# Kernel optimization log

Measured on AMD Instinct MI355X. Metric: run time of the kernel, lower is better.

## Reference

```python
import jax, jax.numpy as jnp
import numpy as np

N = 50000      # number of nodes in batch
K = 32         # padded max neighbors
D = 100        # emb_dim
V = 500000     # n_items
LAYERS = 2


def setup_inputs() -> dict:
    key = jax.random.key(0)
    ks = jax.random.split(key, 9)
    nodes = jax.random.randint(ks[0], (N,), 0, V)
    nei = jax.random.randint(ks[1], (N, K), 0, V)          # padded neighbor ids (pad = 0)
    wei = jax.random.uniform(ks[2], (N, K), dtype=jnp.float32)  # edge weights (pad = 0 in real data)
    s_vec = jax.random.normal(ks[3], (N, D), dtype=jnp.float32)
    emb = jax.random.normal(ks[4], (V, D), dtype=jnp.float32) * 0.02
    emb = emb.at[0].set(0.0)                               # padding_idx=0
    W1_w = jax.random.normal(ks[5], (D + 1, D), dtype=jnp.float32) / np.sqrt(D + 1).astype(np.float32)
    W1_b = jnp.zeros((D,), dtype=jnp.float32)
    q1_w = jax.random.normal(ks[6], (D,), dtype=jnp.float32) / np.sqrt(D).astype(np.float32)
    W2_w = jax.random.normal(ks[7], (2 * D, D), dtype=jnp.float32) / np.sqrt(2 * D).astype(np.float32)
    W2_b = jnp.zeros((D,), dtype=jnp.float32)
    return {"nodes": nodes, "nei": nei, "wei": wei, "s_vec": s_vec,
            "emb": emb, "W1_w": W1_w, "W1_b": W1_b, "q1_w": q1_w,
            "W2_w": W2_w, "W2_b": W2_b}


def reference(nodes, nei, wei, s_vec, emb, W1_w, W1_b, q1_w, W2_w, W2_b):
    # x: [N, D] embeddings of the batch nodes
    x = emb[nodes]
    # In the torch code nei/wei are rebuilt identically every layer and h_nei always
    # comes from the frozen embedding table, so the attention message `msg` is
    # layer-invariant; compute it once (same math as the original loop).
    h_nei = emb[nei]                                              # [N, K, D]
    feat = jnp.concatenate([h_nei * s_vec[:, None, :], wei[..., None]], axis=-1)  # [N, K, D+1]
    score = jnp.einsum('nkd,d->nk', jnp.tanh(feat @ W1_w + W1_b), q1_w)           # [N, K]
    att = jax.nn.softmax(score, axis=-1)                          # no masking, as in original
    msg = jnp.einsum('nk,nkd->nd', att, h_nei)                    # [N, D]
    for _ in range(LAYERS):
        x = jax.nn.relu(jnp.concatenate([x, msg], axis=-1) @ W2_w + W2_b)
    return x
```

## Files before the change

kernel.cpp:

```cpp
#include <hip/hip_runtime.h>
#include <cstdint>
#include <cstddef>

typedef __attribute__((ext_vector_type(8))) short bf16x8;
typedef __attribute__((ext_vector_type(16))) float f32x16;

__device__ __forceinline__ unsigned short f2bf(float f) {
    unsigned int u = __builtin_bit_cast(unsigned int, f);
    u += 0x7fffu + ((u >> 16) & 1u);
    return (unsigned short)(u >> 16);
}

__device__ __forceinline__ unsigned int pk2(float a, float b) {
#if __has_builtin(__builtin_amdgcn_cvt_pk_bf16_f32)
    auto r = __builtin_amdgcn_cvt_pk_bf16_f32(a, b);
    return __builtin_bit_cast(unsigned int, r);
#else
    return (unsigned int)f2bf(a) | ((unsigned int)f2bf(b) << 16);
#endif
}

template<int CTRL>
__device__ __forceinline__ float dpp_add(float v) {
    int t = __builtin_amdgcn_update_dpp(0, __builtin_bit_cast(int, v), CTRL, 0xf, 0xf, true);
    return v + __builtin_bit_cast(float, t);
}

__device__ __forceinline__ float fast_tanh(float x) {
    float e = __expf(2.0f * x);
    return 1.0f - 2.0f / (e + 1.0f);
}

__global__ void prep_kernel(const float* __restrict__ W1, const float* __restrict__ W2,
                            unsigned short* __restrict__ W1t, unsigned short* __restrict__ W2t)
{
    int idx = blockIdx.x * 256 + threadIdx.x;
    if (idx < 128 * 128) {
        int nn = idx >> 7, kk = idx & 127;
        W1t[idx] = (nn < 100 && kk < 100) ? f2bf(W1[kk * 100 + nn]) : (unsigned short)0;
    } else {
        int j = idx - 128 * 128;
        if (j < 128 * 208) {
            int nn = j / 208, kk = j - nn * 208;
            unsigned short v = 0;
            if (nn < 100) {
                if (kk < 100) v = f2bf(W2[kk * 100 + nn]);
                else if (kk >= 104 && kk < 204) v = f2bf(W2[(kk - 4) * 100 + nn]);
            }
            W2t[j] = v;
        }
    }
}

#define HP 104
#define P2P 104

__global__ __launch_bounds__(256) void fused_kernel(
    const int* __restrict__ nodes, const int* __restrict__ nei,
    const float* __restrict__ wei, const float* __restrict__ s_vec,
    const float* __restrict__ emb, const float* __restrict__ W1,
    const float* __restrict__ b1, const float* __restrict__ q1,
    const unsigned short* __restrict__ W1t, const unsigned short* __restrict__ W2t,
    const float* __restrict__ b2, float* __restrict__ out, int N)
{
    __shared__ __align__(16) unsigned short h_s[32 * HP];
    __shared__ __align__(16) unsigned short hst[14 * 32 * 8];
    __shared__ __align__(16) unsigned short msg_s[32 * HP];
    __shared__ __align__(16) float part2[16 * P2P];
    __shared__ __align__(16) float spart[4 * 32];
    __shared__ __align__(16) float wei_s[32];

    const int tid  = threadIdx.x;
    const int lane = tid & 63;
    const int w    = tid >> 6;
    const int col  = lane & 31;
    const int hi   = lane >> 5;
    const int n    = w * 32 + col;
    const int n0   = blockIdx.x * 32;

    bf16x8 Bf1[7];
    #pragma unroll
    for (int ks = 0; ks < 7; ++ks)
        Bf1[ks] = *(const bf16x8*)(W1t + n * 128 + ks * 16 + hi * 8);
    const bool nok   = (n < 100);
    const float b1v  = nok ? b1[n] : 0.0f;
    const float w100 = nok ? W1[100 * 100 + n] : 0.0f;
    const float q1v  = nok ? q1[n] : 0.0f;

    if (tid < 32) {
        *(uint2*)&hst[(12 * 32 + tid) * 8 + 4] = make_uint2(0, 0);
        *(uint4*)&hst[(13 * 32 + tid) * 8]     = make_uint4(0, 0, 0, 0);
        *(uint2*)&h_s[tid * HP + 100]          = make_uint2(0, 0);
        *(uint2*)&msg_s[tid * HP + 100]        = make_uint2(0, 0);
    }
    __syncthreads();

    const int gk = tid >> 3;
    const int gj = tid & 7;

    int   nidx_nx = 0;
    float wv_nx   = 0.0f;
    if (n0 < N) {
        nidx_nx = nei[(size_t)n0 * 32 + gk];
        if (tid < 32) wv_nx = wei[(size_t)n0 * 32 + tid];
    }

    for (int it = 0; it < 32; ++it) {
        const int node = n0 + it;
        if (node >= N) break;
        const int   nidx = nidx_nx;
        const float wv   = wv_nx;
        if (it + 1 < 32 && node + 1 < N) {
            nidx_nx = nei[(size_t)(node + 1) * 32 + gk];
            if (tid < 32) wv_nx = wei[(size_t)(node + 1) * 32 + tid];
        }

        {
            if (tid < 32) wei_s[tid] = wv;
            const float4* erow = (const float4*)(emb + (size_t)nidx * 100);
            const float4* srow = (const float4*)(s_vec + (size_t)node * 100);
            float4 h0 = erow[gj],      s0 = srow[gj];
            float4 h1 = erow[gj + 8],  s1 = srow[gj + 8];
            float4 h2 = erow[gj + 16], s2 = srow[gj + 16];
            float4 h3, s3;
            const bool t24 = (gj == 0);
            if (t24) { h3 = erow[24]; s3 = srow[24]; }
            #define ST_C4(c4, h4, s4) { \
                *(uint2*)&h_s[gk * HP + (c4) * 4] = \
                    make_uint2(pk2(h4.x, h4.y), pk2(h4.z, h4.w)); \
                *(uint2*)&hst[(((c4) >> 1) * 32 + gk) * 8 + ((c4) & 1) * 4] = \
                    make_uint2(pk2(h4.x * s4.x, h4.y * s4.y), pk2(h4.z * s4.z, h4.w * s4.w)); }
            ST_C4(gj,      h0, s0)
            ST_C4(gj + 8,  h1, s1)
            ST_C4(gj + 16, h2, s2)
            if (t24) { ST_C4(24, h3, s3) }
            #undef ST_C4
        }
        __syncthreads();

        f32x16 acc;
        #pragma unroll
        for (int q = 0; q < 4; ++q) {
            float4 wq = *(const float4*)&wei_s[q * 8 + hi * 4];
            acc[q * 4 + 0] = fmaf(wq.x, w100, b1v);
            acc[q * 4 + 1] = fmaf(wq.y, w100, b1v);
            acc[q * 4 + 2] = fmaf(wq.z, w100, b1v);
            acc[q * 4 + 3] = fmaf(wq.w, w100, b1v);
        }
        #pragma unroll
        for (int ks = 0; ks < 7; ++ks) {
            bf16x8 a = *(const bf16x8*)&hst[((2 * ks + hi) * 32 + col) * 8];
            acc = __builtin_amdgcn_mfma_f32_32x32x16_bf16(a, Bf1[ks], acc, 0, 0, 0);
        }

        float sv[16];
        #pragma unroll
        for (int r = 0; r < 16; ++r) sv[r] = fast_tanh(acc[r]) * q1v;
        #pragma unroll
        for (int r = 0; r < 16; ++r) {
            float v = sv[r];
            v = dpp_add<0x111>(v);
            v = dpp_add<0x112>(v);
            v = dpp_add<0x114>(v);
            v = dpp_add<0x118>(v);
            v = dpp_add<0x142>(v);
            sv[r] = v;
        }
        if (col == 31) {
            #pragma unroll
            for (int q = 0; q < 4; ++q)
                *(float4*)&spart[w * 32 + q * 8 + hi * 4] =
                    make_float4(sv[q * 4], sv[q * 4 + 1], sv[q * 4 + 2], sv[q * 4 + 3]);
        }
        __syncthreads();

        float attk;
        {
            float s = spart[col] + spart[32 + col] + spart[64 + col] + spart[96 + col];
            float mx = s;
            #pragma unroll
            for (int off = 16; off; off >>= 1) mx = fmaxf(mx, __shfl_xor(mx, off));
            float e = __expf(s - mx);
            float den = e;
            #pragma unroll
            for (int off = 16; off; off >>= 1) den += __shfl_xor(den, off);
            float attv = e / den;
            attk = __shfl(attv, w * 8 + (lane >> 3));
        }

        {
            const int oct  = lane & 7;
            const int krow = w * 8 + (lane >> 3);
            const float a  = attk;
            uint4 r1 = *(const uint4*)&h_s[krow * HP + oct * 8];
            const int oct2 = (oct < 5) ? oct : 4;
            uint4 r2 = *(const uint4*)&h_s[krow * HP + 64 + oct2 * 8];
            float m1[8], m2[8];
            #define UNP2(u, d0, d1) { d0 = __builtin_bit_cast(float, (u) << 16); \
                                      d1 = __builtin_bit_cast(float, (u) & 0xffff0000u); }
            { float t0,t1; UNP2(r1.x,t0,t1); m1[0]=a*t0; m1[1]=a*t1; }
            { float t0,t1; UNP2(r1.y,t0,t1); m1[2]=a*t0; m1[3]=a*t1; }
            { float t0,t1; UNP2(r1.z,t0,t1); m1[4]=a*t0; m1[5]=a*t1; }
            { float t0,t1; UNP2(r1.w,t0,t1); m1[6]=a*t0; m1[7]=a*t1; }
            { float t0,t1; UNP2(r2.x,t0,t1); m2[0]=a*t0; m2[1]=a*t1; }
            { float t0,t1; UNP2(r2.y,t0,t1); m2[2]=a*t0; m2[3]=a*t1; }
            { float t0,t1; UNP2(r2.z,t0,t1); m2[4]=a*t0; m2[5]=a*t1; }
            { float t0,t1; UNP2(r2.w,t0,t1); m2[6]=a*t0; m2[7]=a*t1; }
            #undef UNP2
            #pragma unroll
            for (int j = 0; j < 8; ++j) {
                m1[j] = dpp_add<0x128>(m1[j]);
                m2[j] = dpp_add<0x128>(m2[j]);
            }
            if ((lane & 8) == 0) {
                const int slot = w * 4 + (lane >> 4);
                float* p = &part2[slot * P2P];
                *(float4*)&p[oct * 8]     = make_float4(m1[0], m1[1], m1[2], m1[3]);
                *(float4*)&p[oct * 8 + 4] = make_float4(m1[4], m1[5], m1[6], m1[7]);
                if (oct < 5) {
                    *(float4*)&p[64 + oct * 8]     = make_float4(m2[0], m2[1], m2[2], m2[3]);
                    *(float4*)&p[64 + oct * 8 + 4] = make_float4(m2[4], m2[5], m2[6], m2[7]);
                }
            }
        }
        __syncthreads();

        if (w < 2) {
            int d = w * 64 + lane;
            if (d < 100) {
                float s = 0.0f;
                #pragma unroll
                for (int sl = 0; sl < 16; ++sl) s += part2[sl * P2P + d];
                msg_s[it * HP + d] = f2bf(s);
            }
        }
    }

    __syncthreads();

    bf16x8 Bf2[13];
    #pragma unroll
    for (int ks = 0; ks < 13; ++ks)
        Bf2[ks] = *(const bf16x8*)(W2t + n * 208 + ks * 16 + hi * 8);
    const float b2v = nok ? b2[n] : 0.0f;
    {
        int row = n0 + gk;
        int rc = row < N ? row : N - 1;
        const float4* xr = (const float4*)(emb + (size_t)nodes[rc] * 100);
        float4 x0 = xr[gj], x1 = xr[gj + 8], x2 = xr[gj + 16];
        float4 x3; const bool t24 = (gj == 0);
        if (t24) x3 = xr[24];
        *(uint2*)&h_s[gk * HP + gj * 4]        = make_uint2(pk2(x0.x, x0.y), pk2(x0.z, x0.w));
        *(uint2*)&h_s[gk * HP + (gj + 8) * 4]  = make_uint2(pk2(x1.x, x1.y), pk2(x1.z, x1.w));
        *(uint2*)&h_s[gk * HP + (gj + 16) * 4] = make_uint2(pk2(x2.x, x2.y), pk2(x2.z, x2.w));
        if (t24)
            *(uint2*)&h_s[gk * HP + 96]        = make_uint2(pk2(x3.x, x3.y), pk2(x3.z, x3.w));
    }
    __syncthreads();

    #define AFRAG(ks) (*(const bf16x8*)( \
        (ks) < 6  ? &h_s[col * HP + (ks) * 16 + hi * 8] : \
        (ks) == 6 ? (hi ? &msg_s[col * HP] : &h_s[col * HP + 96]) : \
                    &msg_s[col * HP + (ks) * 16 + hi * 8 - 104]))

    f32x16 acc;
    #pragma unroll
    for (int r = 0; r < 16; ++r) acc[r] = b2v;
    #pragma unroll
    for (int ks = 0; ks < 13; ++ks)
        acc = __builtin_amdgcn_mfma_f32_32x32x16_bf16(AFRAG(ks), Bf2[ks], acc, 0, 0, 0);
    __syncthreads();
    if (nok) {
        #pragma unroll
        for (int r = 0; r < 16; ++r) {
            int m = (r & 3) + 8 * (r >> 2) + 4 * hi;
            h_s[m * HP + n] = f2bf(fmaxf(acc[r], 0.0f));
        }
    }
    __syncthreads();

    f32x16 acc2;
    #pragma unroll
    for (int r = 0; r < 16; ++r) acc2[r] = b2v;
    #pragma unroll
    for (int ks = 0; ks < 13; ++ks)
        acc2 = __builtin_amdgcn_mfma_f32_32x32x16_bf16(AFRAG(ks), Bf2[ks], acc2, 0, 0, 0);
    #undef AFRAG
    if (nok) {
        #pragma unroll
        for (int r = 0; r < 16; ++r) {
            int m = (r & 3) + 8 * (r >> 2) + 4 * hi;
            int row = n0 + m;
            if (row < N) out[(size_t)row * 100 + n] = fmaxf(acc2[r], 0.0f);
        }
    }
}

extern "C" void kernel_launch(void* const* d_in, const int* in_sizes, int n_in,
                              void* d_out, int out_size, void* d_ws, size_t ws_size,
                              hipStream_t stream) {
    const int*   nodes = (const int*)d_in[0];
    const int*   nei   = (const int*)d_in[1];
    const float* wei   = (const float*)d_in[2];
    const float* s_vec = (const float*)d_in[3];
    const float* emb   = (const float*)d_in[4];
    const float* W1    = (const float*)d_in[5];
    const float* b1    = (const float*)d_in[6];
    const float* q1    = (const float*)d_in[7];
    const float* W2    = (const float*)d_in[8];
    const float* b2    = (const float*)d_in[9];
    float* out = (float*)d_out;
    const int N = in_sizes[0];

    unsigned short* W1t = (unsigned short*)d_ws;
    unsigned short* W2t = W1t + 128 * 128;

    prep_kernel<<<168, 256, 0, stream>>>(W1, W2, W1t, W2t);
    const int gB = (N + 31) / 32;
    fused_kernel<<<gB, 256, 0, stream>>>(nodes, nei, wei, s_vec, emb, W1, b1, q1,
                                         W1t, W2t, b2, out, N);
}
```

Baseline: 678.5 us.

## Prefetch next node's neighbor rows into registers and swap MFMA operands for in-lane score reduction

Gathered embedding and s_vec rows for the next node are now loaded into registers during the current iteration, so the global gather overlaps with the attention compute instead of stalling at the start of each iteration. The W1 MFMA operands are swapped so each lane holds scores for one neighbor, which turns the score reduction into an in-lane FMA chain plus a single cross-half shuffle. Message partials are reduced further with swizzle and shuffle steps, so only four LDS slots are written and summed instead of sixteen. The cost is higher register pressure from the prefetched float4s and the per-row bias, weight and q1 arrays, which may reduce occupancy.

```diff
diff --git a/kernel.cpp b/kernel.cpp
--- a/kernel.cpp
+++ b/kernel.cpp
@@ -23,6 +23,11 @@
 template<int CTRL>
 __device__ __forceinline__ float dpp_add(float v) {
     int t = __builtin_amdgcn_update_dpp(0, __builtin_bit_cast(int, v), CTRL, 0xf, 0xf, true);
+    return v + __builtin_bit_cast(float, t);
+}
+
+__device__ __forceinline__ float swz16_add(float v) {
+    int t = __builtin_amdgcn_ds_swizzle(__builtin_bit_cast(int, v), 0x401F);
     return v + __builtin_bit_cast(float, t);
 }
 
@@ -53,7 +58,6 @@
 }
 
 #define HP 104
-#define P2P 104
 
 __global__ __launch_bounds__(256) void fused_kernel(
     const int* __restrict__ nodes, const int* __restrict__ nei,
@@ -66,8 +70,8 @@
     __shared__ __align__(16) unsigned short h_s[32 * HP];
     __shared__ __align__(16) unsigned short hst[14 * 32 * 8];
     __shared__ __align__(16) unsigned short msg_s[32 * HP];
-    __shared__ __align__(16) float part2[16 * P2P];
-    __shared__ __align__(16) float spart[4 * 32];
+    __shared__ __align__(16) float part2[4 * 100];
+    __shared__ __align__(16) float spart[128];
     __shared__ __align__(16) float wei_s[32];
 
     const int tid  = threadIdx.x;
@@ -82,10 +86,17 @@
     #pragma unroll
     for (int ks = 0; ks < 7; ++ks)
         Bf1[ks] = *(const bf16x8*)(W1t + n * 128 + ks * 16 + hi * 8);
-    const bool nok   = (n < 100);
-    const float b1v  = nok ? b1[n] : 0.0f;
-    const float w100 = nok ? W1[100 * 100 + n] : 0.0f;
-    const float q1v  = nok ? q1[n] : 0.0f;
+
+    float b1r[16], w100r[16], q1r[16];
+    #pragma unroll
+    for (int r = 0; r < 16; ++r) {
+        int nn = w * 32 + (r & 3) + 8 * (r >> 2) + 4 * hi;
+        bool ok = nn < 100;
+        b1r[r]   = ok ? b1[nn] : 0.0f;
+        w100r[r] = ok ? W1[100 * 100 + nn] : 0.0f;
+        q1r[r]   = ok ? q1[nn] : 0.0f;
+    }
+    const bool nok = (n < 100);
 
     if (tid < 32) {
         *(uint2*)&hst[(12 * 32 + tid) * 8 + 4] = make_uint2(0, 0);
@@ -93,38 +104,33 @@
         *(uint2*)&h_s[tid * HP + 100]          = make_uint2(0, 0);
         *(uint2*)&msg_s[tid * HP + 100]        = make_uint2(0, 0);
     }
-    __syncthreads();
 
     const int gk = tid >> 3;
     const int gj = tid & 7;
-
-    int   nidx_nx = 0;
-    float wv_nx   = 0.0f;
-    if (n0 < N) {
-        nidx_nx = nei[(size_t)n0 * 32 + gk];
-        if (tid < 32) wv_nx = wei[(size_t)n0 * 32 + tid];
-    }
+    const bool t24 = (gj == 0);
+
+    float4 h0, h1, h2, h3, s0, s1, s2, s3;
+    int   nidx_pf = 0;
+    float wv = 0.0f;
+    {
+        int nid0 = nei[(size_t)n0 * 32 + gk];
+        const float4* erow = (const float4*)(emb + (size_t)nid0 * 100);
+        const float4* srow = (const float4*)(s_vec + (size_t)n0 * 100);
+        h0 = erow[gj];      s0 = srow[gj];
+        h1 = erow[gj + 8];  s1 = srow[gj + 8];
+        h2 = erow[gj + 16]; s2 = srow[gj + 16];
+        if (t24) { h3 = erow[24]; s3 = srow[24]; }
+        if (tid < 32) wv = wei[(size_t)n0 * 32 + tid];
+        if (n0 + 1 < N) nidx_pf = nei[(size_t)(n0 + 1) * 32 + gk];
+    }
+    __syncthreads();
 
     for (int it = 0; it < 32; ++it) {
         const int node = n0 + it;
         if (node >= N) break;
-        const int   nidx = nidx_nx;
-        const float wv   = wv_nx;
-        if (it + 1 < 32 && node + 1 < N) {
-            nidx_nx = nei[(size_t)(node + 1) * 32 + gk];
-            if (tid < 32) wv_nx = wei[(size_t)(node + 1) * 32 + tid];
-        }
-
+
+        if (tid < 32) wei_s[tid] = wv;
         {
-            if (tid < 32) wei_s[tid] = wv;
-            const float4* erow = (const float4*)(emb + (size_t)nidx * 100);
-            const float4* srow = (const float4*)(s_vec + (size_t)node * 100);
-            float4 h0 = erow[gj],      s0 = srow[gj];
-            float4 h1 = erow[gj + 8],  s1 = srow[gj + 8];
-            float4 h2 = erow[gj + 16], s2 = srow[gj + 16];
-            float4 h3, s3;
-            const bool t24 = (gj == 0);
-            if (t24) { h3 = erow[24]; s3 = srow[24]; }
             #define ST_C4(c4, h4, s4) { \
                 *(uint2*)&h_s[gk * HP + (c4) * 4] = \
                     make_uint2(pk2(h4.x, h4.y), pk2(h4.z, h4.w)); \
@@ -136,42 +142,33 @@
             if (t24) { ST_C4(24, h3, s3) }
             #undef ST_C4
         }
+        if (it + 1 < 32 && node + 1 < N) {
+            const float4* erow = (const float4*)(emb + (size_t)nidx_pf * 100);
+            const float4* srow = (const float4*)(s_vec + (size_t)(node + 1) * 100);
+            h0 = erow[gj];      s0 = srow[gj];
+            h1 = erow[gj + 8];  s1 = srow[gj + 8];
+            h2 = erow[gj + 16]; s2 = srow[gj + 16];
+            if (t24) { h3 = erow[24]; s3 = srow[24]; }
+            if (tid < 32) wv = wei[(size_t)(node + 1) * 32 + tid];
+            if (it + 2 < 32 && node + 2 < N) nidx_pf = nei[(size_t)(node + 2) * 32 + gk];
+        }
         __syncthreads();
 
+        const float wk = wei_s[col];
         f32x16 acc;
         #pragma unroll
-        for (int q = 0; q < 4; ++q) {
-            float4 wq = *(const float4*)&wei_s[q * 8 + hi * 4];
-            acc[q * 4 + 0] = fmaf(wq.x, w100, b1v);
-            acc[q * 4 + 1] = fmaf(wq.y, w100, b1v);
-            acc[q * 4 + 2] = fmaf(wq.z, w100, b1v);
-            acc[q * 4 + 3] = fmaf(wq.w, w100, b1v);
-        }
+        for (int r = 0; r < 16; ++r) acc[r] = fmaf(wk, w100r[r], b1r[r]);
         #pragma unroll
         for (int ks = 0; ks < 7; ++ks) {
-            bf16x8 a = *(const bf16x8*)&hst[((2 * ks + hi) * 32 + col) * 8];
-            acc = __builtin_amdgcn_mfma_f32_32x32x16_bf16(a, Bf1[ks], acc, 0, 0, 0);
-        }
-
-        float sv[16];
-        #pragma unroll
-        for (int r = 0; r < 16; ++r) sv[r] = fast_tanh(acc[r]) * q1v;
-        #pragma unroll
-        for (int r = 0; r < 16; ++r) {
-            float v = sv[r];
-            v = dpp_add<0x111>(v);
-            v = dpp_add<0x112>(v);
-            v = dpp_add<0x114>(v);
-            v = dpp_add<0x118>(v);
-            v = dpp_add<0x142>(v);
-            sv[r] = v;
-        }
-        if (col == 31) {
-            #pragma unroll
-            for (int q = 0; q < 4; ++q)
-                *(float4*)&spart[w * 32 + q * 8 + hi * 4] =
-                    make_float4(sv[q * 4], sv[q * 4 + 1], sv[q * 4 + 2], sv[q * 4 + 3]);
-        }
+            bf16x8 hfrag = *(const bf16x8*)&hst[((2 * ks + hi) * 32 + col) * 8];
+            acc = __builtin_amdgcn_mfma_f32_32x32x16_bf16(Bf1[ks], hfrag, acc, 0, 0, 0);
+        }
+
+        float part = 0.0f;
+        #pragma unroll
+        for (int r = 0; r < 16; ++r) part = fmaf(fast_tanh(acc[r]), q1r[r], part);
+        part += __shfl_xor(part, 32);
+        if (lane < 32) spart[w * 32 + lane] = part;
         __syncthreads();
 
         float attk;
@@ -212,15 +209,22 @@
                 m1[j] = dpp_add<0x128>(m1[j]);
                 m2[j] = dpp_add<0x128>(m2[j]);
             }
-            if ((lane & 8) == 0) {
-                const int slot = w * 4 + (lane >> 4);
-                float* p = &part2[slot * P2P];
+            #pragma unroll
+            for (int j = 0; j < 8; ++j) {
+                m1[j] = swz16_add(m1[j]);
+                m2[j] = swz16_add(m2[j]);
+            }
+            #pragma unroll
+            for (int j = 0; j < 8; ++j) {
+                m1[j] += __shfl_xor(m1[j], 32);
+                m2[j] += __shfl_xor(m2[j], 32);
+            }
+            if ((lane >> 3) == 0) {
+                float* p = &part2[w * 100];
                 *(float4*)&p[oct * 8]     = make_float4(m1[0], m1[1], m1[2], m1[3]);
                 *(float4*)&p[oct * 8 + 4] = make_float4(m1[4], m1[5], m1[6], m1[7]);
-                if (oct < 5) {
-                    *(float4*)&p[64 + oct * 8]     = make_float4(m2[0], m2[1], m2[2], m2[3]);
-                    *(float4*)&p[64 + oct * 8 + 4] = make_float4(m2[4], m2[5], m2[6], m2[7]);
-                }
+                if (oct < 5) *(float4*)&p[64 + oct * 8]     = make_float4(m2[0], m2[1], m2[2], m2[3]);
+                if (oct < 4) *(float4*)&p[64 + oct * 8 + 4] = make_float4(m2[4], m2[5], m2[6], m2[7]);
             }
         }
         __syncthreads();
@@ -228,9 +232,7 @@
         if (w < 2) {
             int d = w * 64 + lane;
             if (d < 100) {
-                float s = 0.0f;
-                #pragma unroll
-                for (int sl = 0; sl < 16; ++sl) s += part2[sl * P2P + d];
+                float s = part2[d] + part2[100 + d] + part2[200 + d] + part2[300 + d];
                 msg_s[it * HP + d] = f2bf(s);
             }
         }
@@ -248,7 +250,7 @@
         int rc = row < N ? row : N - 1;
         const float4* xr = (const float4*)(emb + (size_t)nodes[rc] * 100);
         float4 x0 = xr[gj], x1 = xr[gj + 8], x2 = xr[gj + 16];
-        float4 x3; const bool t24 = (gj == 0);
+        float4 x3;
         if (t24) x3 = xr[24];
         *(uint2*)&h_s[gk * HP + gj * 4]        = make_uint2(pk2(x0.x, x0.y), pk2(x0.z, x0.w));
         *(uint2*)&h_s[gk * HP + (gj + 8) * 4]  = make_uint2(pk2(x1.x, x1.y), pk2(x1.z, x1.w));
```

Measured after the change: 641.4 us. 1.06x faster.
